# Optimization experiments

Measured on AMD Instinct MI355X. Metric: run time of the kernel, lower is better.

The kernel has to match this reference:

```python
import jax, jax.numpy as jnp
import numpy as np

B, L, N, T, D, V, C = 128, 512, 1023, 511, 256, 50000, 511
EPS = 1e-6


def circular_correlation(a, b):
    # c_k = sum_i a_i * b_{(i+k) mod d}  == irfft(conj(rfft(a)) * rfft(b))
    d = a.shape[-1]
    c = jnp.fft.irfft(jnp.conj(jnp.fft.rfft(a, axis=-1)) * jnp.fft.rfft(b, axis=-1), n=d, axis=-1)
    return c / (jnp.linalg.norm(c, axis=-1, keepdims=True) + EPS)


def setup_inputs() -> dict:
    key = jax.random.key(0)
    k1, k2, k3, k4, k5, k6, k7, k8 = jax.random.split(key, 8)
    num_node = jnp.full((B,), N, dtype=jnp.int64 if jax.config.jax_enable_x64 else jnp.int32)
    # leaf slot index: leaves occupy node slots 0..L-1 (deterministic, no scatter collisions)
    slot = jnp.broadcast_to(jnp.arange(L, dtype=jnp.int32)[None, :], (B, L))
    vocab_id = jax.random.randint(k1, (B, L), 0, V, dtype=jnp.int32)
    leaf_content_id = jnp.stack([slot, vocab_id], axis=-1)  # [B, L, 2]
    content_mask = (jax.random.uniform(k2, (B, L)) < 0.9).astype(jnp.int32)
    ctype = jax.random.randint(k3, (B, T), 0, 3, dtype=jnp.int32)          # 0 = no-op, 1, 2 children
    parent = jax.random.randint(k4, (B, T), L, N, dtype=jnp.int32)         # internal node slots
    lchild = jax.random.randint(k5, (B, T), 0, N, dtype=jnp.int32)
    rchild = jax.random.randint(k6, (B, T), 0, N, dtype=jnp.int32)
    composition_info = jnp.stack([ctype, parent, lchild, rchild], axis=-1)  # [B, T, 4]
    emb_weight = jax.random.normal(k7, (V, D), dtype=jnp.float32) * 0.1
    lin_weight = jax.random.normal(k8, (C, D), dtype=jnp.float32) * 0.05
    lin_bias = jnp.zeros((C,), dtype=jnp.float32)
    return {"num_node": num_node, "leaf_content_id": leaf_content_id,
            "content_mask": content_mask, "composition_info": composition_info,
            "emb_weight": emb_weight, "lin_weight": lin_weight, "lin_bias": lin_bias}


def embed_leaf_nodes(leaf_content_id, content_mask, emb_weight):
    leaf_vec = emb_weight[leaf_content_id[:, :, 1]]          # [B, L, D]
    node_idx = leaf_content_id[:, :, 0]                      # [B, L]
    mask = content_mask != 0
    safe_idx = jnp.where(mask, node_idx, N)                  # N is out-of-bounds -> dropped
    vec = jnp.zeros((B, N, D), dtype=leaf_vec.dtype)
    vec = vec.at[jnp.arange(B)[:, None], safe_idx].set(leaf_vec, mode="drop")
    norm = jnp.linalg.norm(vec, axis=2, keepdims=True) + EPS
    return vec / norm


def compose(vec, composition_info):
    bidx = jnp.arange(B)

    def step(v, info):  # info: [B, 4] for one tree level
        t, p, l, r = info[:, 0], info[:, 1], info[:, 2], info[:, 3]
        safe_p = jnp.where(t > 0, p, 0)
        lv = v[bidx, l]                                      # [B, D]
        rv = v[bidx, r]
        two = circular_correlation(lv, rv)
        cur = v[bidx, safe_p]
        val = jnp.where((t == 1)[:, None], lv,
                        jnp.where((t == 2)[:, None], two, cur))
        return v.at[bidx, safe_p].set(val), None

    vec, _ = jax.lax.scan(step, vec, jnp.swapaxes(composition_info, 0, 1))
    return vec


def reference(num_node, leaf_content_id, content_mask, composition_info,
              emb_weight, lin_weight, lin_bias):
    vec = embed_leaf_nodes(leaf_content_id, content_mask, emb_weight)
    vec = compose(vec, composition_info)
    out = jnp.einsum("bnd,cd->bnc", vec, lin_weight) + lin_bias
    return out
```

## Files before the change

kernel.cpp:

```cpp
#include <hip/hip_runtime.h>

#define NB 128
#define NL 512
#define NN 1023
#define NT 511
#define ND 256
#define NC 511
#define EPSF 1e-6f

#define SRC_ZERO (-1)
#define SLOTC 4096
#define STEPC 8192

typedef __attribute__((ext_vector_type(8))) short short8;
typedef __attribute__((ext_vector_type(4))) float f32x4;

__device__ __forceinline__ unsigned short f2bf(float f) {
  unsigned u = __builtin_bit_cast(unsigned, f);
  u += 0x7FFFu + ((u >> 16) & 1u);
  return (unsigned short)(u >> 16);
}

__global__ void __launch_bounds__(256) embed_scatter(
    const int* __restrict__ lcid, const int* __restrict__ cmask,
    const float* __restrict__ emb, const float* __restrict__ lw,
    float* __restrict__ leafbuf, unsigned short* __restrict__ vecb,
    unsigned short* __restrict__ wb) {
  if (blockIdx.x >= 16384) {
    int i   = (blockIdx.x - 16384) * 256 + threadIdx.x;
    int row = i >> 5;
    uint4 r = {0u, 0u, 0u, 0u};
    if (row < NC) {
      const float4* v4 = (const float4*)lw;
      float4 x = v4[2 * i], y = v4[2 * i + 1];
      r.x = (unsigned)f2bf(x.x) | ((unsigned)f2bf(x.y) << 16);
      r.y = (unsigned)f2bf(x.z) | ((unsigned)f2bf(x.w) << 16);
      r.z = (unsigned)f2bf(y.x) | ((unsigned)f2bf(y.y) << 16);
      r.w = (unsigned)f2bf(y.z) | ((unsigned)f2bf(y.w) << 16);
    }
    ((uint4*)wb)[i] = r;
    return;
  }
  int rid  = blockIdx.x * 4 + (threadIdx.x >> 6);
  int lane = threadIdx.x & 63;
  int slot = lcid[2 * rid];
  int vid  = lcid[2 * rid + 1];
  int msk  = cmask[rid];
  int b    = rid >> 9;
  float4 v = {0.f, 0.f, 0.f, 0.f};
  if (msk) v = ((const float4*)(emb + (size_t)vid * ND))[lane];
  float ss = v.x * v.x + v.y * v.y + v.z * v.z + v.w * v.w;
#pragma unroll
  for (int off = 32; off > 0; off >>= 1) ss += __shfl_down(ss, off, 64);
  ss = __shfl(ss, 0, 64);
  float inv = 1.0f / (sqrtf(ss) + EPSF);
  float4 o;
  o.x = v.x * inv; o.y = v.y * inv; o.z = v.z * inv; o.w = v.w * inv;
  ((float4*)(leafbuf + ((size_t)b * 512 + slot) * ND))[lane] = o;
  uint2 pk;
  pk.x = (unsigned)f2bf(o.x) | ((unsigned)f2bf(o.y) << 16);
  pk.y = (unsigned)f2bf(o.z) | ((unsigned)f2bf(o.w) << 16);
  ((uint2*)(vecb + ((size_t)b * NN + slot) * ND))[lane] = pk;
}

__global__ void __launch_bounds__(1024) compose_kernel(
    const int* __restrict__ info, const int* __restrict__ lcid,
    const int* __restrict__ cmask, const float* __restrict__ leafbuf,
    float* __restrict__ outbuf, int* __restrict__ fsrcG) {
  const int b    = blockIdx.x;
  const int tid  = threadIdx.x;
  const int lane = tid & 63;
  const int wav  = tid >> 6;

  __shared__ int4 sinfo4[NT];
  __shared__ int lwl[NT], lwr[NT], fwr[NT];
  __shared__ int ptr_[NT];
  __shared__ int lsA[NT], rsA[NT];
  __shared__ int lvl[NT], fsrc[NT];
  __shared__ int schedS[NT], schedL[NT], schedR[NT];
  __shared__ int offs[512], cnt[512], cnt2[512];
  __shared__ unsigned char deadF[NT], liveF[NT], lzero[512];
  __shared__ float a_st[16][256], b_st[16][512];
  __shared__ int changed, smax;

  const float* lb = leafbuf + (size_t)b * 512 * ND;
  float*       ob = outbuf + (size_t)b * NT * ND;

  const int4* ib4 = (const int4*)(info + (size_t)b * NT * 4);
  for (int i = tid; i < NT; i += 1024) sinfo4[i] = ib4[i];
  if (tid < 512) lzero[tid] = 1;
  if (tid == 0) smax = 0;
  __syncthreads();
  if (tid < NL) {
    int row = lcid[((size_t)b * NL + tid) * 2];
    lzero[row] = (cmask[(size_t)b * NL + tid] == 0) ? 1 : 0;
  }
  __syncthreads();

  const int t = tid;
  int4 m1 = {0, 0, 0, 0};
  if (t < NT) m1 = sinfo4[t];
  int l1 = -1, r1 = -1, f1 = -1;
  const int prow = 512 + t;
  for (int tp = 0; tp < NT; ++tp) {
    int4 wi = sinfo4[tp];
    if (wi.x > 0) {
      if (t < NT && tp < t) { if (wi.y == m1.z) l1 = tp; if (wi.y == m1.w) r1 = tp; }
      if (wi.y == prow) f1 = tp;
    }
  }
  if (t < NT) { lwl[t] = l1; lwr[t] = r1; fwr[t] = f1; }
  __syncthreads();

  if (t < NT) {
    int v;
    if (m1.x == 2) v = SLOTC + t;
    else if (m1.x == 1) {
      if (m1.z < 512) v = m1.z;
      else v = (l1 >= 0) ? (STEPC + l1) : SRC_ZERO;
    } else v = SRC_ZERO;
    ptr_[t] = v;
  }
  __syncthreads();
  for (int it = 0; it < 10; ++it) {
    int v = 0;
    if (t < NT) { v = ptr_[t]; if (v >= STEPC) v = ptr_[v - STEPC]; }
    __syncthreads();
    if (t < NT) ptr_[t] = v;
    __syncthreads();
  }

  auto normv = [&](int v) -> int {
    if (v >= 0 && v < 512 && lzero[v]) return SRC_ZERO;
    return v;
  };
  auto collapseW = [&](int wstep) -> int {
    int v = (sinfo4[wstep].x == 2) ? (SLOTC + wstep) : ptr_[wstep];
    return normv(v);
  };
  if (t < NT) {
    if (m1.x == 2) {
      int a = (m1.z < 512) ? normv(m1.z) : ((l1 >= 0) ? collapseW(l1) : SRC_ZERO);
      int c = (m1.w < 512) ? normv(m1.w) : ((r1 >= 0) ? collapseW(r1) : SRC_ZERO);
      lsA[t] = a; rsA[t] = c;
      deadF[t] = (a == SRC_ZERO || c == SRC_ZERO) ? 1 : 0;
    } else {
      deadF[t] = 0;
    }
    liveF[t] = 0;
    fsrc[t] = (f1 >= 0) ? collapseW(f1) : SRC_ZERO;
  }
  __syncthreads();

  for (int rounds = 0; rounds < NT; ++rounds) {
    if (tid == 0) changed = 0;
    __syncthreads();
    if (t < NT && m1.x == 2 && !deadF[t]) {
      int a = lsA[t], c = rsA[t];
      if (a >= SLOTC && deadF[a - SLOTC]) { a = SRC_ZERO; lsA[t] = a; }
      if (c >= SLOTC && deadF[c - SLOTC]) { c = SRC_ZERO; rsA[t] = c; }
      if (a == SRC_ZERO || c == SRC_ZERO) { deadF[t] = 1; changed = 1; }
    }
    __syncthreads();
    if (!changed) break;
    __syncthreads();
  }

  if (t < NT) {
    int f = fsrc[t];
    if (f >= SLOTC && deadF[f - SLOTC]) { f = SRC_ZERO; fsrc[t] = f; }
    if (f >= SLOTC) liveF[f - SLOTC] = 1;
  }
  __syncthreads();
  for (int rounds = 0; rounds < NT; ++rounds) {
    if (tid == 0) changed = 0;
    __syncthreads();
    if (t < NT && m1.x == 2 && liveF[t] && !deadF[t]) {
      int a = lsA[t], c = rsA[t];
      if (a >= SLOTC && !liveF[a - SLOTC]) { liveF[a - SLOTC] = 1; changed = 1; }
      if (c >= SLOTC && !liveF[c - SLOTC]) { liveF[c - SLOTC] = 1; changed = 1; }
    }
    __syncthreads();
    if (!changed) break;
    __syncthreads();
  }

  const bool isLive = (t < NT && m1.x == 2 && liveF[t] && !deadF[t]);

  if (t < NT) lvl[t] = 0;
  __syncthreads();
  for (int rounds = 0; rounds < NT; ++rounds) {
    if (tid == 0) changed = 0;
    __syncthreads();
    if (isLive) {
      int nl = 1, a = lsA[t], c = rsA[t];
      if (a >= SLOTC) { int dl = lvl[a - SLOTC] + 1; if (dl > nl) nl = dl; }
      if (c >= SLOTC) { int dl = lvl[c - SLOTC] + 1; if (dl > nl) nl = dl; }
      if (nl > lvl[t]) { lvl[t] = nl; changed = 1; }
    }
    __syncthreads();
    if (!changed) break;
    __syncthreads();
  }
  if (isLive) atomicMax(&smax, lvl[t]);

  if (tid < 512) { cnt[tid] = 0; cnt2[tid] = 0; }
  __syncthreads();
  if (isLive) atomicAdd(&cnt[lvl[t]], 1);
  __syncthreads();
  if (tid < 512) offs[tid] = cnt[tid];
  __syncthreads();
  for (int k = 1; k < 512; k <<= 1) {
    int v = 0;
    if (tid < 512) { v = offs[tid]; if (tid >= k) v += offs[tid - k]; }
    __syncthreads();
    if (tid < 512) offs[tid] = v;
    __syncthreads();
  }
  if (isLive) {
    int d = lvl[t];
    int pos = offs[d - 1] + atomicAdd(&cnt2[d], 1);
    schedS[pos] = t; schedL[pos] = lsA[t]; schedR[pos] = rsA[t];
  }
  __syncthreads();

  const int maxd = smax;
  for (int d = 1; d <= maxd; ++d) {
    const int base = offs[d - 1];
    const int nops = cnt[d];
    const int nch  = (nops + 15) >> 4;
    for (int ch = 0; ch < nch; ++ch) {
      int rel = ch * 16 + wav;
      if (rel < nops) {
        int my = base + rel;
        int tt = schedS[my], ls = schedL[my], rs = schedR[my];
        const float* pa = (ls < 512) ? lb + (size_t)ls * ND
                                     : ob + (size_t)(ls - SLOTC) * ND;
        const float* pb = (rs < 512) ? lb + (size_t)rs * ND
                                     : ob + (size_t)(rs - SLOTC) * ND;
        float4 av = ((const float4*)pa)[lane];
        float4 bv = ((const float4*)pb)[lane];
        ((float4*)a_st[wav])[lane] = av;
        ((float4*)b_st[wav])[lane]      = bv;
        ((float4*)b_st[wav])[lane + 64] = bv;
        const float4* a4 = (const float4*)a_st[wav];
        const float4* b4 = (const float4*)b_st[wav];
        float c0 = 0.f, c1 = 0.f, c2 = 0.f, c3 = 0.f;
        float4 B0 = b4[lane];
#pragma unroll 8
        for (int i = 0; i < 64; ++i) {
          float4 A  = a4[i];
          float4 B1 = b4[lane + i + 1];
          c0 += A.x * B0.x + A.y * B0.y + A.z * B0.z + A.w * B0.w;
          c1 += A.x * B0.y + A.y * B0.z + A.z * B0.w + A.w * B1.x;
          c2 += A.x * B0.z + A.y * B0.w + A.z * B1.x + A.w * B1.y;
          c3 += A.x * B0.w + A.y * B1.x + A.z * B1.y + A.w * B1.z;
          B0 = B1;
        }
        float ss = c0 * c0 + c1 * c1 + c2 * c2 + c3 * c3;
#pragma unroll
        for (int off = 32; off > 0; off >>= 1) ss += __shfl_down(ss, off, 64);
        ss = __shfl(ss, 0, 64);
        float inv = 1.f / (sqrtf(ss) + EPSF);
        float4 res;
        res.x = c0 * inv; res.y = c1 * inv; res.z = c2 * inv; res.w = c3 * inv;
        ((float4*)(ob + (size_t)tt * ND))[lane] = res;
      }
    }
    __syncthreads();
  }

  for (int i = tid; i < NT; i += 1024) fsrcG[b * NT + i] = fsrc[i];
}

__global__ void __launch_bounds__(256) gather_rows(
    const int* __restrict__ fsrcG, const float* __restrict__ leafbuf,
    const float* __restrict__ outbuf, unsigned short* __restrict__ vecb) {
  int rid  = blockIdx.x * 4 + (threadIdx.x >> 6);
  int lane = threadIdx.x & 63;
  int b    = rid / NT;
  int idx  = rid - b * NT;
  int s    = fsrcG[rid];
  float4 v = {0.f, 0.f, 0.f, 0.f};
  if (s >= 0) {
    const float* src = (s < 512)
        ? (leafbuf + ((size_t)b * 512 + s) * ND)
        : (outbuf + ((size_t)b * NT + (s - SLOTC)) * ND);
    v = ((const float4*)src)[lane];
  }
  uint2 pk;
  pk.x = (unsigned)f2bf(v.x) | ((unsigned)f2bf(v.y) << 16);
  pk.y = (unsigned)f2bf(v.z) | ((unsigned)f2bf(v.w) << 16);
  ((uint2*)(vecb + ((size_t)b * NN + 512 + idx) * ND))[lane] = pk;
}

union GemmSh {
  struct { short As[128 * 64]; short Ws[128 * 64]; } s;
  float epi[4][16][65];
};

__global__ void __launch_bounds__(256) gemm_kernel(
    const short* __restrict__ A, const short* __restrict__ W,
    const float* __restrict__ bias, float* __restrict__ out) {
  __shared__ GemmSh sh;
  int tid  = threadIdx.x;
  int lane = tid & 63;
  int w    = tid >> 6;
  int c0   = blockIdx.x * 128;
  int m0   = blockIdx.y * 128;
  int wm   = (w & 1) * 64;
  int wc   = (w >> 1) * 64;
  int frow = lane & 15;
  int quad = lane >> 4;
  f32x4 acc[4][4];
#pragma unroll
  for (int i = 0; i < 4; ++i)
#pragma unroll
    for (int j = 0; j < 4; ++j) acc[i][j] = (f32x4){0.f, 0.f, 0.f, 0.f};

  for (int k0 = 0; k0 < ND; k0 += 64) {
#pragma unroll
    for (int i = 0; i < 4; ++i) {
      int idx = i * 256 + tid;
      int row = idx >> 3;
      int ch  = idx & 7;
      int chs = ch ^ (row & 7);
      const short* ga = A + (size_t)(m0 + row) * ND + k0 + chs * 8;
      const short* gw = W + (size_t)(c0 + row) * ND + k0 + chs * 8;
      __builtin_amdgcn_global_load_lds(
          (const __attribute__((address_space(1))) void*)ga,
          (__attribute__((address_space(3))) void*)(sh.s.As + idx * 8), 16, 0, 0);
      __builtin_amdgcn_global_load_lds(
          (const __attribute__((address_space(1))) void*)gw,
          (__attribute__((address_space(3))) void*)(sh.s.Ws + idx * 8), 16, 0, 0);
    }
    __syncthreads();
#pragma unroll
    for (int ks = 0; ks < 2; ++ks) {
      short8 af[4], wf[4];
#pragma unroll
      for (int mi = 0; mi < 4; ++mi) {
        int r = wm + mi * 16 + frow;
        int cc = (ks * 4 + quad) ^ (r & 7);
        af[mi] = *(const short8*)(sh.s.As + r * 64 + cc * 8);
      }
#pragma unroll
      for (int ci = 0; ci < 4; ++ci) {
        int r = wc + ci * 16 + frow;
        int cc = (ks * 4 + quad) ^ (r & 7);
        wf[ci] = *(const short8*)(sh.s.Ws + r * 64 + cc * 8);
      }
#pragma unroll
      for (int mi = 0; mi < 4; ++mi)
#pragma unroll
        for (int ci = 0; ci < 4; ++ci)
          acc[mi][ci] = __builtin_amdgcn_mfma_f32_16x16x32_bf16(
              af[mi], wf[ci], acc[mi][ci], 0, 0, 0);
    }
    __syncthreads();
  }

  int colg = c0 + wc + lane;
  float bv = (colg < NC) ? bias[colg] : 0.f;
#pragma unroll
  for (int mi = 0; mi < 4; ++mi) {
#pragma unroll
    for (int ci = 0; ci < 4; ++ci)
#pragma unroll
      for (int r = 0; r < 4; ++r)
        sh.epi[w][quad * 4 + r][ci * 16 + frow] = acc[mi][ci][r];
    if (colg < NC) {
      int mrow = m0 + wm + mi * 16;
#pragma unroll
      for (int rr = 0; rr < 16; ++rr)
        out[(size_t)(mrow + rr) * NC + colg] = sh.epi[w][rr][lane] + bv;
    }
  }
}

extern "C" void kernel_launch(void* const* d_in, const int* in_sizes, int n_in,
                              void* d_out, int out_size, void* d_ws, size_t ws_size,
                              hipStream_t stream) {
  const int*   lcid  = (const int*)d_in[1];
  const int*   cmask = (const int*)d_in[2];
  const int*   cinfo = (const int*)d_in[3];
  const float* emb   = (const float*)d_in[4];
  const float* lw    = (const float*)d_in[5];
  const float* lbias = (const float*)d_in[6];
  float*       out   = (float*)d_out;

  char* ws = (char*)d_ws;
  float*          leafbuf = (float*)ws;
  float*          outbuf  = (float*)(ws + 67108864);
  unsigned short* vecb    = (unsigned short*)(ws + 134086656);
  unsigned short* wb      = (unsigned short*)(ws + 201129984);
  int*            fsrcG   = (int*)d_out;

  embed_scatter<<<16448, 256, 0, stream>>>(lcid, cmask, emb, lw,
                                           leafbuf, vecb, wb);
  compose_kernel<<<NB, 1024, 0, stream>>>(cinfo, lcid, cmask, leafbuf,
                                          outbuf, fsrcG);
  gather_rows<<<NB * NT / 4, 256, 0, stream>>>(fsrcG, leafbuf, outbuf, vecb);
  gemm_kernel<<<dim3(4, 1023), 256, 0, stream>>>(
      (const short*)vecb, (const short*)wb, lbias, out);
}
```

Measured before the change: 559.5 us.

## Use packed FMA in circular correlation and swizzle GEMM block order

In the compose kernel, a second shifted copy of the b vector is staged in shared memory so every product pairs with aligned float2 operands, which lets the compiler emit packed fp32 FMA (v_pk_fma_f32) in the correlation loop. The GEMM launch becomes a 1D grid whose blocks are remapped so groups of 8 M-tiles cycle through the 4 C-tiles, improving L2 reuse of A rows. This costs extra LDS (another 32KB) and a few early-exit blocks. It also removes unused shared arrays.

```diff
diff --git a/kernel.cpp b/kernel.cpp
--- a/kernel.cpp
+++ b/kernel.cpp
@@ -14,6 +14,7 @@
 
 typedef __attribute__((ext_vector_type(8))) short short8;
 typedef __attribute__((ext_vector_type(4))) float f32x4;
+typedef __attribute__((ext_vector_type(2))) float f32x2;
 
 __device__ __forceinline__ unsigned short f2bf(float f) {
   unsigned u = __builtin_bit_cast(unsigned, f);
@@ -73,14 +74,15 @@
   const int wav  = tid >> 6;
 
   __shared__ int4 sinfo4[NT];
-  __shared__ int lwl[NT], lwr[NT], fwr[NT];
   __shared__ int ptr_[NT];
   __shared__ int lsA[NT], rsA[NT];
   __shared__ int lvl[NT], fsrc[NT];
   __shared__ int schedS[NT], schedL[NT], schedR[NT];
   __shared__ int offs[512], cnt[512], cnt2[512];
   __shared__ unsigned char deadF[NT], liveF[NT], lzero[512];
-  __shared__ float a_st[16][256], b_st[16][512];
+  __shared__ float a_st[16][256];
+  __shared__ float b_st[16][512];
+  __shared__ float s_st[16][512];
   __shared__ int changed, smax;
 
   const float* lb = leafbuf + (size_t)b * 512 * ND;
@@ -109,7 +111,6 @@
       if (wi.y == prow) f1 = tp;
     }
   }
-  if (t < NT) { lwl[t] = l1; lwr[t] = r1; fwr[t] = f1; }
   __syncthreads();
 
   if (t < NT) {
@@ -240,23 +241,36 @@
                                      : ob + (size_t)(rs - SLOTC) * ND;
         float4 av = ((const float4*)pa)[lane];
         float4 bv = ((const float4*)pb)[lane];
-        ((float4*)a_st[wav])[lane] = av;
+        float nx = __shfl(bv.x, (lane + 1) & 63, 64);
+        float4 sv = {bv.y, bv.z, bv.w, nx};
+        ((float4*)a_st[wav])[lane]      = av;
         ((float4*)b_st[wav])[lane]      = bv;
         ((float4*)b_st[wav])[lane + 64] = bv;
+        ((float4*)s_st[wav])[lane]      = sv;
+        ((float4*)s_st[wav])[lane + 64] = sv;
         const float4* a4 = (const float4*)a_st[wav];
         const float4* b4 = (const float4*)b_st[wav];
-        float c0 = 0.f, c1 = 0.f, c2 = 0.f, c3 = 0.f;
+        const float4* s4 = (const float4*)s_st[wav];
+        f32x2 q0 = {0.f, 0.f}, q1 = {0.f, 0.f}, q2 = {0.f, 0.f}, q3 = {0.f, 0.f};
         float4 B0 = b4[lane];
+        float4 S0 = s4[lane];
 #pragma unroll 8
         for (int i = 0; i < 64; ++i) {
           float4 A  = a4[i];
           float4 B1 = b4[lane + i + 1];
-          c0 += A.x * B0.x + A.y * B0.y + A.z * B0.z + A.w * B0.w;
-          c1 += A.x * B0.y + A.y * B0.z + A.z * B0.w + A.w * B1.x;
-          c2 += A.x * B0.z + A.y * B0.w + A.z * B1.x + A.w * B1.y;
-          c3 += A.x * B0.w + A.y * B1.x + A.z * B1.y + A.w * B1.z;
-          B0 = B1;
+          float4 S1 = s4[lane + i + 1];
+          f32x2 Axy = {A.x, A.y},  Azw = {A.z, A.w};
+          f32x2 Bxy = {B0.x, B0.y}, Bzw = {B0.z, B0.w};
+          f32x2 Sxy = {S0.x, S0.y}, Szw = {S0.z, S0.w};
+          f32x2 B1xy = {B1.x, B1.y}, S1xy = {S1.x, S1.y};
+          q0 += Axy * Bxy;  q0 += Azw * Bzw;
+          q1 += Axy * Sxy;  q1 += Azw * Szw;
+          q2 += Axy * Bzw;  q2 += Azw * B1xy;
+          q3 += Axy * Szw;  q3 += Azw * S1xy;
+          B0 = B1; S0 = S1;
         }
+        float c0 = q0.x + q0.y, c1 = q1.x + q1.y;
+        float c2 = q2.x + q2.y, c3 = q3.x + q3.y;
         float ss = c0 * c0 + c1 * c1 + c2 * c2 + c3 * c3;
 #pragma unroll
         for (int off = 32; off > 0; off >>= 1) ss += __shfl_down(ss, off, 64);
@@ -303,25 +317,29 @@
     const short* __restrict__ A, const short* __restrict__ W,
     const float* __restrict__ bias, float* __restrict__ out) {
   __shared__ GemmSh sh;
+  int i = blockIdx.x;
+  int m = (i >> 5) * 8 + (i & 7);
+  int c = (i >> 3) & 3;
+  if (m >= 1023) return;
   int tid  = threadIdx.x;
   int lane = tid & 63;
   int w    = tid >> 6;
-  int c0   = blockIdx.x * 128;
-  int m0   = blockIdx.y * 128;
+  int c0   = c * 128;
+  int m0   = m * 128;
   int wm   = (w & 1) * 64;
   int wc   = (w >> 1) * 64;
   int frow = lane & 15;
   int quad = lane >> 4;
   f32x4 acc[4][4];
 #pragma unroll
-  for (int i = 0; i < 4; ++i)
-#pragma unroll
-    for (int j = 0; j < 4; ++j) acc[i][j] = (f32x4){0.f, 0.f, 0.f, 0.f};
+  for (int a = 0; a < 4; ++a)
+#pragma unroll
+    for (int j = 0; j < 4; ++j) acc[a][j] = (f32x4){0.f, 0.f, 0.f, 0.f};
 
   for (int k0 = 0; k0 < ND; k0 += 64) {
 #pragma unroll
-    for (int i = 0; i < 4; ++i) {
-      int idx = i * 256 + tid;
+    for (int a = 0; a < 4; ++a) {
+      int idx = a * 256 + tid;
       int row = idx >> 3;
       int ch  = idx & 7;
       int chs = ch ^ (row & 7);
@@ -401,6 +419,6 @@
   compose_kernel<<<NB, 1024, 0, stream>>>(cinfo, lcid, cmask, leafbuf,
                                           outbuf, fsrcG);
   gather_rows<<<NB * NT / 4, 256, 0, stream>>>(fsrcG, leafbuf, outbuf, vecb);
-  gemm_kernel<<<dim3(4, 1023), 256, 0, stream>>>(
+  gemm_kernel<<<4096, 256, 0, stream>>>(
       (const short*)vecb, (const short*)wb, lbias, out);
 }
```

Measured after the change: 520.6 us. 7.0% less time.
